# Performance work log

Hardware: AMD Instinct MI355X
Metric: run time of the kernel (lower is better)

The kernel has to match this reference:

```python
import jax, jax.numpy as jnp
import numpy as np

B, L, D, H = 2, 1000, 288, 8
DIM = D // H          # 36 per-head dim
DFF = 2 * D           # 576 conv-FFN hidden
KS = L // 4           # 250 sampled keys per query
NQ = L // 4           # 250 selected (active) queries
EPS = 1e-5


def _layernorm(x, g, b):
    mu = x.mean(-1, keepdims=True)
    var = ((x - mu) ** 2).mean(-1, keepdims=True)
    return (x - mu) * jax.lax.rsqrt(var + EPS) * g + b


def _prob_attention(q, k, v, index_key):
    # q,k,v: [b,h,L,dim]; index_key: [L, KS]
    b, h, l, dim = q.shape
    # sample KS keys per query row (gather): [b,h,L,KS,dim]
    k_samp = jnp.take(k, index_key, axis=2)
    # sampled scores: [b,h,L,KS]
    scores_samp = jnp.einsum('bhld,bhlkd->bhlk', q, k_samp)
    # sparsity measure M(q) = max - mean(over full l_key, as in source)
    measure = scores_samp.max(-1) - scores_samp.sum(-1) / l
    # top-NQ active queries per (b,h): [b,h,NQ]
    idx_q = jax.lax.top_k(measure, NQ)[1]
    q_sel = jnp.take_along_axis(q, idx_q[..., None], axis=2)  # [b,h,NQ,dim]
    sim = jnp.einsum('bhqd,bhkd->bhqk', q_sel, k) * (1.0 / np.sqrt(dim))
    attn = jax.nn.softmax(sim, axis=-1)
    out_sel = jnp.einsum('bhqk,bhkd->bhqd', attn, v)          # [b,h,NQ,dim]
    # lazy queries get mean(V); scatter active outputs in
    out = jnp.broadcast_to(v.mean(axis=2, keepdims=True), v.shape)
    bi = jnp.arange(b)[:, None, None]
    hi = jnp.arange(h)[None, :, None]
    out = out.at[bi, hi, idx_q].set(out_sel)
    return out  # [b,h,L,dim]


def reference(x, index_key, Wq, bq, Wk, bk, Wv, bv, W1, b1, W2, b2,
              ln1_g, ln1_b, ln2_g, ln2_b):
    b, l, d = x.shape
    # QKV projections -> [b,h,L,dim]
    q = (x @ Wq.T + bq).reshape(b, l, H, DIM).transpose(0, 2, 1, 3)
    k = (x @ Wk.T + bk).reshape(b, l, H, DIM).transpose(0, 2, 1, 3)
    v = (x @ Wv.T + bv).reshape(b, l, H, DIM).transpose(0, 2, 1, 3)
    attn = _prob_attention(q, k, v, index_key)
    attn = attn.transpose(0, 2, 1, 3).reshape(b, l, d)
    # residual + LN1 (dropout is identity in eval)
    h1 = _layernorm(x + attn, ln1_g, ln1_b)
    # conv FFN (kernel_size=1 conv == per-position linear), exact GELU
    f = jax.nn.gelu(h1 @ W1.T + b1, approximate=False)   # [b,l,DFF]
    f = jax.nn.gelu(f @ W2.T + b2, approximate=False)    # [b,l,d]
    return _layernorm(f + h1, ln2_g, ln2_b)


def setup_inputs() -> dict:
    key = jax.random.key(0)
    ks = jax.random.split(key, 10)
    s = 0.05
    return {
        'x': jax.random.normal(ks[0], (B, L, D), jnp.float32),
        'index_key': jax.random.randint(ks[1], (L, KS), 0, L),
        'Wq': jax.random.normal(ks[2], (D, D), jnp.float32) * s,
        'bq': jnp.zeros((D,), jnp.float32),
        'Wk': jax.random.normal(ks[3], (D, D), jnp.float32) * s,
        'bk': jnp.zeros((D,), jnp.float32),
        'Wv': jax.random.normal(ks[4], (D, D), jnp.float32) * s,
        'bv': jnp.zeros((D,), jnp.float32),
        'W1': jax.random.normal(ks[5], (DFF, D), jnp.float32) * s,
        'b1': jnp.zeros((DFF,), jnp.float32),
        'W2': jax.random.normal(ks[6], (D, DFF), jnp.float32) * s,
        'b2': jnp.zeros((D,), jnp.float32),
        'ln1_g': jnp.ones((D,), jnp.float32),
        'ln1_b': jnp.zeros((D,), jnp.float32),
        'ln2_g': jnp.ones((D,), jnp.float32),
        'ln2_b': jnp.zeros((D,), jnp.float32),
    }
```

## Files before the change

kernel.cpp:

```cpp
#include <hip/hip_runtime.h>
#include <math.h>

#define B_ 2
#define L_ 1000
#define D_ 288
#define H_ 8
#define DIM_ 36
#define DFF_ 576
#define KS_ 250
#define NQ_ 250
#define BH_ (B_ * H_)
#define EPS_ 1e-5f
#define PSTRIDE_ 40
#define MAXCL_ 125

__device__ __forceinline__ float gelu_exact(float x) {
    return 0.5f * x * (1.0f + erff(x * 0.70710678118654752f));
}

__device__ __forceinline__ float dot4(float4 a, float4 b) {
    return a.x * b.x + a.y * b.y + a.z * b.z + a.w * b.w;
}

__global__ __launch_bounds__(256) void qkv_transpose_kernel(
    const float* __restrict__ Wq, const float* __restrict__ Wk,
    const float* __restrict__ Wv,
    float* __restrict__ WqT, float* __restrict__ WkT, float* __restrict__ WvT)
{
    __shared__ float tile[32][33];
    const int m = blockIdx.x / 81;
    const int t = blockIdx.x % 81;
    const float* src = (m == 0) ? Wq : (m == 1) ? Wk : Wv;
    float* dst = (m == 0) ? WqT : (m == 1) ? WkT : WvT;
    const int ty0 = (t / 9) * 32, tx0 = (t % 9) * 32;
    const int tx = threadIdx.x & 31, ty = threadIdx.x >> 5;
#pragma unroll
    for (int i = 0; i < 4; i++)
        tile[ty + 8 * i][tx] = src[(size_t)(ty0 + ty + 8 * i) * D_ + tx0 + tx];
    __syncthreads();
#pragma unroll
    for (int i = 0; i < 4; i++)
        dst[(size_t)(tx0 + ty + 8 * i) * D_ + ty0 + tx] = tile[tx][ty + 8 * i];
}

__global__ __launch_bounds__(256) void ffn_transpose_kernel(
    const float* __restrict__ W1, const float* __restrict__ W2,
    float* __restrict__ W1T, float* __restrict__ W2T)
{
    __shared__ float tile[32][33];
    int t = blockIdx.x;
    const float* src; float* dst; int Rr, Cc, ntx;
    if (t < 162) { src = W1; dst = W1T; Rr = DFF_; Cc = D_; ntx = 9; }
    else { t -= 162; src = W2; dst = W2T; Rr = D_; Cc = DFF_; ntx = 18; }
    const int ty0 = (t / ntx) * 32, tx0 = (t % ntx) * 32;
    const int tx = threadIdx.x & 31, ty = threadIdx.x >> 5;
#pragma unroll
    for (int i = 0; i < 4; i++)
        tile[ty + 8 * i][tx] = src[(size_t)(ty0 + ty + 8 * i) * Cc + tx0 + tx];
    __syncthreads();
#pragma unroll
    for (int i = 0; i < 4; i++)
        dst[(size_t)(tx0 + ty + 8 * i) * Rr + ty0 + tx] = tile[tx][ty + 8 * i];
}

__global__ __launch_bounds__(256) void qkvT2_kernel(
    const float* __restrict__ x,
    const float* __restrict__ WqT, const float* __restrict__ WkT,
    const float* __restrict__ WvT,
    const float* __restrict__ bq, const float* __restrict__ bk,
    const float* __restrict__ bv,
    float* __restrict__ Q, float* __restrict__ K, float* __restrict__ V,
    float* __restrict__ KT)
{
    __shared__ float xsT[D_][4];
    const int base = blockIdx.x * 4;
    const int tid = threadIdx.x;

    for (int idx = tid; idx < 4 * D_; idx += 256) {
        int r = idx / D_, k = idx % D_;
        xsT[k][r] = x[(size_t)(base + r) * D_ + k];
    }
    __syncthreads();

    if (tid < 216) {
        const int gcol = 4 * tid;
        const int m = gcol / D_;
        const int c = gcol - m * D_;
        const float* WT = (m == 0) ? WqT : (m == 1) ? WkT : WvT;
        const float* bias = (m == 0) ? bq : (m == 1) ? bk : bv;
        float* outp = (m == 0) ? Q : (m == 1) ? K : V;

        float a[4][4];
#pragma unroll
        for (int j = 0; j < 4; j++) {
            float bv2 = bias[c + j];
#pragma unroll
            for (int r = 0; r < 4; r++) a[j][r] = bv2;
        }

        for (int k = 0; k < D_; k++) {
            float4 w = *(const float4*)(WT + (size_t)k * D_ + c);
            float4 xv = *(const float4*)&xsT[k][0];
            a[0][0] += w.x * xv.x; a[0][1] += w.x * xv.y; a[0][2] += w.x * xv.z; a[0][3] += w.x * xv.w;
            a[1][0] += w.y * xv.x; a[1][1] += w.y * xv.y; a[1][2] += w.y * xv.z; a[1][3] += w.y * xv.w;
            a[2][0] += w.z * xv.x; a[2][1] += w.z * xv.y; a[2][2] += w.z * xv.z; a[2][3] += w.z * xv.w;
            a[3][0] += w.w * xv.x; a[3][1] += w.w * xv.y; a[3][2] += w.w * xv.z; a[3][3] += w.w * xv.w;
        }

        const int bb_ = base / L_;
        const int l0 = base % L_;
#pragma unroll
        for (int j = 0; j < 4; j++) {
            int col = c + j;
            int h = col / DIM_, dd = col % DIM_;
#pragma unroll
            for (int r = 0; r < 4; r++) {
                int row = base + r;
                int b = row / L_, l = row % L_;
                outp[((size_t)(b * H_ + h) * L_ + l) * DIM_ + dd] = a[j][r];
            }
            if (m == 1) {
                *(float4*)(KT + ((size_t)(bb_ * H_ + h) * DIM_ + dd) * L_ + l0) =
                    make_float4(a[j][0], a[j][1], a[j][2], a[j][3]);
            }
        }
    }
}

__global__ __launch_bounds__(320) void qkv_kernel(
    const float* __restrict__ x,
    const float* __restrict__ Wq, const float* __restrict__ bq,
    const float* __restrict__ Wk, const float* __restrict__ bk,
    const float* __restrict__ Wv, const float* __restrict__ bv,
    float* __restrict__ Q, float* __restrict__ K, float* __restrict__ V)
{
    constexpr int R = 8;
    __shared__ float xs[R][D_];
    const int base = blockIdx.x * R;
    const int tid = threadIdx.x;

    const float4* xsrc = (const float4*)(x + (size_t)base * D_);
    float4* xdst = (float4*)&xs[0][0];
    for (int i = tid; i < R * D_ / 4; i += 320) xdst[i] = xsrc[i];
    __syncthreads();

    if (tid < D_) {
        const float4* wq4 = (const float4*)(Wq + (size_t)tid * D_);
        const float4* wk4 = (const float4*)(Wk + (size_t)tid * D_);
        const float4* wv4 = (const float4*)(Wv + (size_t)tid * D_);
        float aq[R], ak[R], av[R];
        float biasq = bq[tid], biask = bk[tid], biasv = bv[tid];
#pragma unroll
        for (int r = 0; r < R; r++) { aq[r] = biasq; ak[r] = biask; av[r] = biasv; }
        for (int d4 = 0; d4 < D_ / 4; d4++) {
            float4 wqv = wq4[d4], wkv = wk4[d4], wvv = wv4[d4];
#pragma unroll
            for (int r = 0; r < R; r++) {
                float4 hv = *(const float4*)&xs[r][d4 * 4];
                aq[r] += dot4(hv, wqv);
                ak[r] += dot4(hv, wkv);
                av[r] += dot4(hv, wvv);
            }
        }
        const int h = tid / DIM_, dd = tid % DIM_;
#pragma unroll
        for (int r = 0; r < R; r++) {
            int row = base + r;
            int b = row / L_, l = row % L_;
            size_t o = ((size_t)(b * H_ + h) * L_ + l) * DIM_ + dd;
            Q[o] = aq[r]; K[o] = ak[r]; V[o] = av[r];
        }
    }
}

__global__ __launch_bounds__(256) void score_measure3_kernel(
    const float* __restrict__ Q, const float* __restrict__ KT,
    const int* __restrict__ index_key, float* __restrict__ measure)
{
    constexpr int R = 8;
    __shared__ float qs[R][DIM_];
    __shared__ float st[R][1004];
    const int bh = blockIdx.x / 125;
    const int qt = blockIdx.x % 125;
    const int tid = threadIdx.x;

    if (tid < R * DIM_ / 4)
        ((float4*)&qs[0][0])[tid] =
            ((const float4*)(Q + ((size_t)bh * L_ + qt * R) * DIM_))[tid];
    __syncthreads();

    const float* KTb = KT + (size_t)bh * DIM_ * L_;
#pragma unroll
    for (int i = 0; i < 4; i++) {
        const int k = i * 256 + tid;
        if (k < L_) {
            float acc[R];
#pragma unroll
            for (int r = 0; r < R; r++) acc[r] = 0.f;
#pragma unroll
            for (int d4 = 0; d4 < DIM_ / 4; d4++) {
                float4 kv;
                kv.x = KTb[(size_t)(d4 * 4 + 0) * L_ + k];
                kv.y = KTb[(size_t)(d4 * 4 + 1) * L_ + k];
                kv.z = KTb[(size_t)(d4 * 4 + 2) * L_ + k];
                kv.w = KTb[(size_t)(d4 * 4 + 3) * L_ + k];
#pragma unroll
                for (int r = 0; r < R; r++)
                    acc[r] += dot4(*(const float4*)&qs[r][d4 * 4], kv);
            }
#pragma unroll
            for (int r = 0; r < R; r++) st[r][k] = acc[r];
        }
    }
    __syncthreads();

    const int r = tid >> 5;
    const int lane = tid & 31;
    const int l = qt * R + r;
    const int* ik = index_key + l * KS_;
    float mx = -1e30f, sm = 0.f;
    for (int s = lane; s < KS_; s += 32) {
        float v = st[r][ik[s]];
        mx = fmaxf(mx, v);
        sm += v;
    }
#pragma unroll
    for (int off = 16; off; off >>= 1) {
        mx = fmaxf(mx, __shfl_xor(mx, off));
        sm += __shfl_xor(sm, off);
    }
    if (lane == 0) measure[bh * L_ + l] = mx - sm * (1.0f / (float)L_);
}

__global__ __launch_bounds__(256) void measure_kernel(
    const float* __restrict__ Q, const float* __restrict__ K,
    const int* __restrict__ index_key, float* __restrict__ measure)
{
    const int w = threadIdx.x >> 6;
    const int lane = threadIdx.x & 63;
    const int wid = blockIdx.x * 4 + w;
    const int bh = wid / L_;
    const int l = wid % L_;

    const float4* qp = (const float4*)(Q + ((size_t)bh * L_ + l) * DIM_);
    float4 q[9];
#pragma unroll
    for (int i = 0; i < 9; i++) q[i] = qp[i];

    const int* ik = index_key + l * KS_;
    const float* Kb = K + (size_t)bh * L_ * DIM_;

    float mx = -1e30f, sm = 0.f;
#pragma unroll
    for (int s = lane; s < KS_; s += 64) {
        int kidx = ik[s];
        const float4* k4 = (const float4*)(Kb + (size_t)kidx * DIM_);
        float acc = 0.f;
#pragma unroll
        for (int i = 0; i < 9; i++) acc += dot4(q[i], k4[i]);
        mx = fmaxf(mx, acc);
        sm += acc;
    }
#pragma unroll
    for (int off = 32; off; off >>= 1) {
        mx = fmaxf(mx, __shfl_xor(mx, off));
        sm += __shfl_xor(sm, off);
    }
    if (lane == 0) measure[wid] = mx - sm * (1.0f / (float)L_);
}

__global__ __launch_bounds__(256) void topk_vmean_kernel(
    const float* __restrict__ measure, int* __restrict__ qlist,
    int* __restrict__ slot_map, const float* __restrict__ V,
    float* __restrict__ Vmean)
{
    if (blockIdx.x < BH_ * 4) {
        const int bh = blockIdx.x >> 2;
        const int quarter = blockIdx.x & 3;
        __shared__ float m[L_];
        for (int i = threadIdx.x; i < L_; i += 256) m[i] = measure[bh * L_ + i];
        __syncthreads();
        const int i = quarter * 250 + threadIdx.x;
        if (threadIdx.x < 250) {
            float mi = m[i];
            int rank = 0;
            for (int j = 0; j < L_; j++) {
                float mj = m[j];
                rank += (mj > mi) || (mj == mi && j < i);
            }
            if (rank < NQ_) qlist[bh * NQ_ + rank] = i;
            slot_map[bh * L_ + i] = (rank < NQ_) ? rank : -1;
        }
    } else {
        const int bh = blockIdx.x - BH_ * 4;
        const int tid = threadIdx.x;
        __shared__ float red2[7][DIM_];
        if (tid < 252) {
            int gq = tid / DIM_, d = tid % DIM_;
            const float* basep = V + (size_t)bh * L_ * DIM_;
            float s = 0.f;
            for (int l = gq; l < L_; l += 7) s += basep[l * DIM_ + d];
            red2[gq][d] = s;
        }
        __syncthreads();
        if (tid < DIM_) {
            float s = 0.f;
#pragma unroll
            for (int gq = 0; gq < 7; gq++) s += red2[gq][tid];
            Vmean[bh * DIM_ + tid] = s * (1.0f / L_);
        }
    }
}

__global__ __launch_bounds__(256) void attn_part2_kernel(
    const float* __restrict__ Q, const float* __restrict__ K,
    const float* __restrict__ V, const int* __restrict__ qlist,
    float* __restrict__ part, int nchunk, int chunk_len)
{
    __shared__ float Ks[MAXCL_ * DIM_];
    __shared__ float Vs[MAXCL_ * DIM_];
    const int bh = blockIdx.x / nchunk;
    const int chunk = blockIdx.x % nchunk;
    const int tid = threadIdx.x;
    const int k0 = chunk * chunk_len;

    {
        const float4* Ksrc = (const float4*)(K + ((size_t)bh * L_ + k0) * DIM_);
        const float4* Vsrc = (const float4*)(V + ((size_t)bh * L_ + k0) * DIM_);
        const int nf4 = chunk_len * (DIM_ / 4);
        for (int i = tid; i < nf4; i += 256) {
            ((float4*)Ks)[i] = Ksrc[i];
            ((float4*)Vs)[i] = Vsrc[i];
        }
    }
    __syncthreads();

    const int slot = tid;
    if (slot >= NQ_) return;

    const int qidx = qlist[bh * NQ_ + slot];
    const float4* qp = (const float4*)(Q + ((size_t)bh * L_ + qidx) * DIM_);
    float4 q[9];
#pragma unroll
    for (int i = 0; i < 9; i++) q[i] = qp[i];

    const float scale = (float)(1.0 / 6.0);
    float4 acc[9];
#pragma unroll
    for (int i = 0; i < 9; i++) acc[i] = make_float4(0.f, 0.f, 0.f, 0.f);
    float sum = 0.f;

    for (int j = 0; j < chunk_len; j++) {
        const float4* kp = (const float4*)(Ks + j * DIM_);
        float s = 0.f;
#pragma unroll
        for (int i = 0; i < 9; i++) s += dot4(q[i], kp[i]);
        float e = __expf(s * scale);
        sum += e;
        const float4* vp = (const float4*)(Vs + j * DIM_);
#pragma unroll
        for (int i = 0; i < 9; i++) {
            float4 vv = vp[i];
            acc[i].x += e * vv.x;
            acc[i].y += e * vv.y;
            acc[i].z += e * vv.z;
            acc[i].w += e * vv.w;
        }
    }

    float* p = part + ((size_t)(bh * NQ_ + slot) * nchunk + chunk) * PSTRIDE_;
#pragma unroll
    for (int i = 0; i < 9; i++) ((float4*)p)[i] = acc[i];
    p[DIM_] = sum;
}

__global__ __launch_bounds__(320) void combine_ln1_kernel(
    const float* __restrict__ x, const float* __restrict__ part,
    const int* __restrict__ slot_map, const float* __restrict__ Vmean,
    const float* __restrict__ g, const float* __restrict__ bb,
    float* __restrict__ h1, int nchunk)
{
    const int row = blockIdx.x;
    const int b = row / L_, l = row % L_;
    const int tid = threadIdx.x;
    __shared__ float psum[5], pssq[5];

    float y = 0.f;
    if (tid < D_) {
        const int h = tid / DIM_, d = tid % DIM_;
        const int bh = b * H_ + h;
        const int slot = slot_map[bh * L_ + l];
        float v;
        if (slot < 0) {
            v = Vmean[bh * DIM_ + d];
        } else {
            const float* p = part + (size_t)(bh * NQ_ + slot) * nchunk * PSTRIDE_;
            float a = 0.f, s = 0.f;
            for (int c = 0; c < nchunk; c++) {
                a += p[c * PSTRIDE_ + d];
                s += p[c * PSTRIDE_ + DIM_];
            }
            v = a / s;
        }
        y = x[(size_t)row * D_ + tid] + v;
    }

    float s1 = y, s2 = y * y;
#pragma unroll
    for (int off = 32; off; off >>= 1) {
        s1 += __shfl_xor(s1, off);
        s2 += __shfl_xor(s2, off);
    }
    const int w = tid >> 6, lane = tid & 63;
    if (lane == 0) { psum[w] = s1; pssq[w] = s2; }
    __syncthreads();
    float ts = 0.f, tq = 0.f;
#pragma unroll
    for (int i = 0; i < 5; i++) { ts += psum[i]; tq += pssq[i]; }
    float mu = ts * (1.0f / D_);
    float var = tq * (1.0f / D_) - mu * mu;
    float rstd = rsqrtf(var + EPS_);
    if (tid < D_)
        h1[(size_t)row * D_ + tid] = (y - mu) * rstd * g[tid] + bb[tid];
}

__global__ __launch_bounds__(288) void ffn_fused3_kernel(
    const float* __restrict__ h1,
    const float* __restrict__ W1T, const float* __restrict__ b1,
    const float* __restrict__ W2T, const float* __restrict__ b2,
    const float* __restrict__ g, const float* __restrict__ bb,
    float* __restrict__ out)
{
    constexpr int R = 8;
    __shared__ float hs[R][D_];
    __shared__ float fs[R][DFF_];
    __shared__ float red[6912];
    __shared__ float ys[R][D_];
    const int base = blockIdx.x * R;
    const int tid = threadIdx.x;

    {
        const float4* src = (const float4*)(h1 + (size_t)base * D_);
        float4* dst = (float4*)&hs[0][0];
        for (int i = tid; i < R * D_ / 4; i += 288) dst[i] = src[i];
    }
    __syncthreads();

    {
        const int kg = tid / 144;
        const int ct = tid - kg * 144;
        const int c = 4 * ct;
        float a[4][R];
#pragma unroll
        for (int j = 0; j < 4; j++) {
            float bv = (kg == 0) ? b1[c + j] : 0.f;
#pragma unroll
            for (int r = 0; r < R; r++) a[j][r] = bv;
        }
        const int kbeg = kg * 144;
        for (int k = kbeg; k < kbeg + 144; k++) {
            float4 w = *(const float4*)(W1T + (size_t)k * DFF_ + c);
#pragma unroll
            for (int r = 0; r < R; r++) {
                float xv = hs[r][k];
                a[0][r] += w.x * xv;
                a[1][r] += w.y * xv;
                a[2][r] += w.z * xv;
                a[3][r] += w.w * xv;
            }
        }
        if (kg == 1) {
#pragma unroll
            for (int j = 0; j < 4; j++) {
                *(float4*)&red[(j * 144 + ct) * 8 + 0] =
                    make_float4(a[j][0], a[j][1], a[j][2], a[j][3]);
                *(float4*)&red[(j * 144 + ct) * 8 + 4] =
                    make_float4(a[j][4], a[j][5], a[j][6], a[j][7]);
            }
        }
        __syncthreads();
        if (kg == 0) {
            float y[4][R];
#pragma unroll
            for (int j = 0; j < 4; j++) {
                float4 o0 = *(const float4*)&red[(j * 144 + ct) * 8 + 0];
                float4 o1 = *(const float4*)&red[(j * 144 + ct) * 8 + 4];
                y[j][0] = gelu_exact(a[j][0] + o0.x);
                y[j][1] = gelu_exact(a[j][1] + o0.y);
                y[j][2] = gelu_exact(a[j][2] + o0.z);
                y[j][3] = gelu_exact(a[j][3] + o0.w);
                y[j][4] = gelu_exact(a[j][4] + o1.x);
                y[j][5] = gelu_exact(a[j][5] + o1.y);
                y[j][6] = gelu_exact(a[j][6] + o1.z);
                y[j][7] = gelu_exact(a[j][7] + o1.w);
            }
#pragma unroll
            for (int r = 0; r < R; r++)
                *(float4*)&fs[r][c] = make_float4(y[0][r], y[1][r], y[2][r], y[3][r]);
        }
    }
    __syncthreads();

    {
        const int kg = tid / 72;
        const int ct = tid - kg * 72;
        const int c = 4 * ct;
        float a[4][R];
#pragma unroll
        for (int j = 0; j < 4; j++) {
            float bv = (kg == 0) ? b2[c + j] : 0.f;
#pragma unroll
            for (int r = 0; r < R; r++) a[j][r] = bv;
        }
        const int kbeg = kg * 144;
        for (int k = kbeg; k < kbeg + 144; k++) {
            float4 w = *(const float4*)(W2T + (size_t)k * D_ + c);
#pragma unroll
            for (int r = 0; r < R; r++) {
                float fv = fs[r][k];
                a[0][r] += w.x * fv;
                a[1][r] += w.y * fv;
                a[2][r] += w.z * fv;
                a[3][r] += w.w * fv;
            }
        }
        if (kg >= 1) {
#pragma unroll
            for (int j = 0; j < 4; j++) {
                *(float4*)&red[(((kg - 1) * 4 + j) * 72 + ct) * 8 + 0] =
                    make_float4(a[j][0], a[j][1], a[j][2], a[j][3]);
                *(float4*)&red[(((kg - 1) * 4 + j) * 72 + ct) * 8 + 4] =
                    make_float4(a[j][4], a[j][5], a[j][6], a[j][7]);
            }
        }
        __syncthreads();
        if (kg == 0) {
            float y[4][R];
#pragma unroll
            for (int j = 0; j < 4; j++) {
#pragma unroll
                for (int rq = 0; rq < 2; rq++) {
                    float4 o0 = *(const float4*)&red[((0 * 4 + j) * 72 + ct) * 8 + rq * 4];
                    float4 o1 = *(const float4*)&red[((1 * 4 + j) * 72 + ct) * 8 + rq * 4];
                    float4 o2 = *(const float4*)&red[((2 * 4 + j) * 72 + ct) * 8 + rq * 4];
                    y[j][rq * 4 + 0] = gelu_exact(a[j][rq * 4 + 0] + o0.x + o1.x + o2.x) + hs[rq * 4 + 0][c + j];
                    y[j][rq * 4 + 1] = gelu_exact(a[j][rq * 4 + 1] + o0.y + o1.y + o2.y) + hs[rq * 4 + 1][c + j];
                    y[j][rq * 4 + 2] = gelu_exact(a[j][rq * 4 + 2] + o0.z + o1.z + o2.z) + hs[rq * 4 + 2][c + j];
                    y[j][rq * 4 + 3] = gelu_exact(a[j][rq * 4 + 3] + o0.w + o1.w + o2.w) + hs[rq * 4 + 3][c + j];
                }
            }
#pragma unroll
            for (int r = 0; r < R; r++)
                *(float4*)&ys[r][c] = make_float4(y[0][r], y[1][r], y[2][r], y[3][r]);
        }
    }
    __syncthreads();

    const int w = tid >> 6;
    const int lane = tid & 63;
    if (w < 4) {
#pragma unroll
        for (int rr = 0; rr < 2; rr++) {
            const int r = w * 2 + rr;
            float s = 0.f, ss = 0.f;
#pragma unroll
            for (int i = 0; i < 5; i++) {
                int j = lane + i * 64;
                if (j < D_) { float yv = ys[r][j]; s += yv; ss += yv * yv; }
            }
#pragma unroll
            for (int off = 32; off; off >>= 1) {
                s += __shfl_xor(s, off);
                ss += __shfl_xor(ss, off);
            }
            float mu = s * (1.0f / D_);
            float var = ss * (1.0f / D_) - mu * mu;
            float rstd = rsqrtf(var + EPS_);
            int row = base + r;
#pragma unroll
            for (int i = 0; i < 5; i++) {
                int j = lane + i * 64;
                if (j < D_)
                    out[(size_t)row * D_ + j] = (ys[r][j] - mu) * rstd * g[j] + bb[j];
            }
        }
    }
}

__global__ __launch_bounds__(192) void ffn1_kernel(
    const float* __restrict__ h1,
    const float* __restrict__ W1, const float* __restrict__ b1,
    float* __restrict__ f1)
{
    constexpr int R = 8;
    __shared__ float hs[R][D_];
    const int base = blockIdx.x * R;
    const int tid = threadIdx.x;

    const float4* hsrc = (const float4*)(h1 + (size_t)base * D_);
    float4* hdst = (float4*)&hs[0][0];
    for (int i = tid; i < R * D_ / 4; i += 192) hdst[i] = hsrc[i];
    __syncthreads();

    const int j0 = tid, j1 = tid + 192, j2 = tid + 384;
    const float4* w0 = (const float4*)(W1 + (size_t)j0 * D_);
    const float4* w1 = (const float4*)(W1 + (size_t)j1 * D_);
    const float4* w2 = (const float4*)(W1 + (size_t)j2 * D_);
    float a0[R], a1[R], a2[R];
    float bb0 = b1[j0], bb1 = b1[j1], bb2 = b1[j2];
#pragma unroll
    for (int r = 0; r < R; r++) { a0[r] = bb0; a1[r] = bb1; a2[r] = bb2; }

    for (int d4 = 0; d4 < D_ / 4; d4++) {
        float4 x0 = w0[d4], x1 = w1[d4], x2 = w2[d4];
#pragma unroll
        for (int r = 0; r < R; r++) {
            float4 hv = *(const float4*)&hs[r][d4 * 4];
            a0[r] += dot4(hv, x0);
            a1[r] += dot4(hv, x1);
            a2[r] += dot4(hv, x2);
        }
    }
#pragma unroll
    for (int r = 0; r < R; r++) {
        size_t rowo = (size_t)(base + r) * DFF_;
        f1[rowo + j0] = gelu_exact(a0[r]);
        f1[rowo + j1] = gelu_exact(a1[r]);
        f1[rowo + j2] = gelu_exact(a2[r]);
    }
}

__global__ __launch_bounds__(320) void ffn2_ln_kernel(
    const float* __restrict__ f1, const float* __restrict__ h1,
    const float* __restrict__ W2, const float* __restrict__ b2,
    const float* __restrict__ g, const float* __restrict__ bb,
    float* __restrict__ out)
{
    constexpr int R = 8;
    __shared__ float fs[R][DFF_];
    __shared__ float hs[R][D_];
    __shared__ float ys[R][D_];
    const int base = blockIdx.x * R;
    const int tid = threadIdx.x;

    const float4* fsrc = (const float4*)(f1 + (size_t)base * DFF_);
    float4* fdst = (float4*)&fs[0][0];
    for (int i = tid; i < R * DFF_ / 4; i += 320) fdst[i] = fsrc[i];
    const float4* hsrc = (const float4*)(h1 + (size_t)base * D_);
    float4* hdst = (float4*)&hs[0][0];
    for (int i = tid; i < R * D_ / 4; i += 320) hdst[i] = hsrc[i];
    __syncthreads();

    if (tid < D_) {
        const float4* w4 = (const float4*)(W2 + (size_t)tid * DFF_);
        float acc[R];
        float bias = b2[tid];
#pragma unroll
        for (int r = 0; r < R; r++) acc[r] = bias;
        for (int d4 = 0; d4 < DFF_ / 4; d4++) {
            float4 wv = w4[d4];
#pragma unroll
            for (int r = 0; r < R; r++) {
                float4 fv = *(const float4*)&fs[r][d4 * 4];
                acc[r] += dot4(fv, wv);
            }
        }
#pragma unroll
        for (int r = 0; r < R; r++) ys[r][tid] = gelu_exact(acc[r]) + hs[r][tid];
    }
    __syncthreads();

    const int w = tid >> 6;
    const int lane = tid & 63;
    for (int r = w; r < R; r += 5) {
        float s = 0.f, ss = 0.f;
#pragma unroll
        for (int i = 0; i < 5; i++) {
            int j = lane + i * 64;
            if (j < D_) { float y = ys[r][j]; s += y; ss += y * y; }
        }
#pragma unroll
        for (int off = 32; off; off >>= 1) {
            s += __shfl_xor(s, off);
            ss += __shfl_xor(ss, off);
        }
        float mu = s * (1.0f / D_);
        float var = ss * (1.0f / D_) - mu * mu;
        float rstd = rsqrtf(var + EPS_);
        int row = base + r;
#pragma unroll
        for (int i = 0; i < 5; i++) {
            int j = lane + i * 64;
            if (j < D_) out[(size_t)row * D_ + j] = (ys[r][j] - mu) * rstd * g[j] + bb[j];
        }
    }
}

extern "C" void kernel_launch(void* const* d_in, const int* in_sizes, int n_in,
                              void* d_out, int out_size, void* d_ws, size_t ws_size,
                              hipStream_t stream)
{
    const float* x         = (const float*)d_in[0];
    const int*   index_key = (const int*)  d_in[1];
    const float* Wq = (const float*)d_in[2];
    const float* bq = (const float*)d_in[3];
    const float* Wk = (const float*)d_in[4];
    const float* bk = (const float*)d_in[5];
    const float* Wv = (const float*)d_in[6];
    const float* bv = (const float*)d_in[7];
    const float* W1 = (const float*)d_in[8];
    const float* b1 = (const float*)d_in[9];
    const float* W2 = (const float*)d_in[10];
    const float* b2 = (const float*)d_in[11];
    const float* ln1_g = (const float*)d_in[12];
    const float* ln1_b = (const float*)d_in[13];
    const float* ln2_g = (const float*)d_in[14];
    const float* ln2_b = (const float*)d_in[15];
    float* out = (float*)d_out;

    float* Q        = (float*)d_ws;
    float* K        = Q + 576000;
    float* V        = K + 576000;
    float* Vmean    = V + 576000;
    float* measure  = Vmean + 576;
    float* attn_out = measure + 16000;
    float* h1       = attn_out + 576000;
    int*   qlist    = (int*)(h1 + 576000);
    int*   slot_map = qlist + 4000;
    float* part     = (float*)(slot_map + 16000);
    float* f1       = part;
    float* KT       = part + 4000000;

    float* WqT = part;
    float* WkT = WqT + 82944;
    float* WvT = WkT + 82944;
    float* W1T = part;
    float* W2T = part + 165888;

    const size_t kt_end = 2916576ull + 4000000ull + 576000ull;
    const bool   big    = ws_size >= kt_end * sizeof(float);
    const int    nchunk = big ? 25 : 8;
    const int    chunk_len = L_ / nchunk;

    if (big) {
        qkv_transpose_kernel<<<243, 256, 0, stream>>>(Wq, Wk, Wv, WqT, WkT, WvT);
        qkvT2_kernel<<<500, 256, 0, stream>>>(x, WqT, WkT, WvT, bq, bk, bv, Q, K, V, KT);
        score_measure3_kernel<<<BH_ * 125, 256, 0, stream>>>(Q, KT, index_key, measure);
    } else {
        qkv_kernel<<<250, 320, 0, stream>>>(x, Wq, bq, Wk, bk, Wv, bv, Q, K, V);
        measure_kernel<<<4000, 256, 0, stream>>>(Q, K, index_key, measure);
    }
    topk_vmean_kernel<<<BH_ * 4 + BH_, 256, 0, stream>>>(measure, qlist, slot_map, V, Vmean);
    attn_part2_kernel<<<BH_ * nchunk, 256, 0, stream>>>(Q, K, V, qlist, part, nchunk, chunk_len);
    combine_ln1_kernel<<<B_ * L_, 320, 0, stream>>>(x, part, slot_map, Vmean,
                                                    ln1_g, ln1_b, h1, nchunk);
    if (big) {
        ffn_transpose_kernel<<<324, 256, 0, stream>>>(W1, W2, W1T, W2T);
        ffn_fused3_kernel<<<250, 288, 0, stream>>>(h1, W1T, b1, W2T, b2, ln2_g, ln2_b, out);
    } else {
        ffn1_kernel<<<250, 192, 0, stream>>>(h1, W1, b1, f1);
        ffn2_ln_kernel<<<250, 320, 0, stream>>>(f1, h1, W2, b2, ln2_g, ln2_b, out);
    }
}
```

Baseline: 273.2 us.

## Merge weight transposes into one launch and split-K the QKV and FFN kernels

All five weight transposes now run in a single prep kernel, and the FFN weights are written to a separate buffer so they are no longer overwritten by the attention partials. The QKV projection splits its K loop across two thread groups (448 threads) and reduces the halves through shared memory. The fused FFN kernel processes 4 rows per block instead of 8, with 576 threads and a 4-way split-K for the first GEMM, giving twice as many blocks. The intent is more parallelism and one fewer launch, at the cost of extra shared-memory reductions, more barriers, and less weight reuse per block.

```diff
diff --git a/kernel.cpp b/kernel.cpp
--- a/kernel.cpp
+++ b/kernel.cpp
@@ -22,48 +22,45 @@
     return a.x * b.x + a.y * b.y + a.z * b.z + a.w * b.w;
 }
 
-__global__ __launch_bounds__(256) void qkv_transpose_kernel(
+__global__ __launch_bounds__(256) void weights_prep_kernel(
     const float* __restrict__ Wq, const float* __restrict__ Wk,
     const float* __restrict__ Wv,
-    float* __restrict__ WqT, float* __restrict__ WkT, float* __restrict__ WvT)
-{
-    __shared__ float tile[32][33];
-    const int m = blockIdx.x / 81;
-    const int t = blockIdx.x % 81;
-    const float* src = (m == 0) ? Wq : (m == 1) ? Wk : Wv;
-    float* dst = (m == 0) ? WqT : (m == 1) ? WkT : WvT;
-    const int ty0 = (t / 9) * 32, tx0 = (t % 9) * 32;
-    const int tx = threadIdx.x & 31, ty = threadIdx.x >> 5;
-#pragma unroll
-    for (int i = 0; i < 4; i++)
-        tile[ty + 8 * i][tx] = src[(size_t)(ty0 + ty + 8 * i) * D_ + tx0 + tx];
-    __syncthreads();
-#pragma unroll
-    for (int i = 0; i < 4; i++)
-        dst[(size_t)(tx0 + ty + 8 * i) * D_ + ty0 + tx] = tile[tx][ty + 8 * i];
-}
-
-__global__ __launch_bounds__(256) void ffn_transpose_kernel(
+    float* __restrict__ WqT, float* __restrict__ WkT, float* __restrict__ WvT,
     const float* __restrict__ W1, const float* __restrict__ W2,
     float* __restrict__ W1T, float* __restrict__ W2T)
 {
     __shared__ float tile[32][33];
-    int t = blockIdx.x;
-    const float* src; float* dst; int Rr, Cc, ntx;
-    if (t < 162) { src = W1; dst = W1T; Rr = DFF_; Cc = D_; ntx = 9; }
-    else { t -= 162; src = W2; dst = W2T; Rr = D_; Cc = DFF_; ntx = 18; }
-    const int ty0 = (t / ntx) * 32, tx0 = (t % ntx) * 32;
     const int tx = threadIdx.x & 31, ty = threadIdx.x >> 5;
-#pragma unroll
-    for (int i = 0; i < 4; i++)
-        tile[ty + 8 * i][tx] = src[(size_t)(ty0 + ty + 8 * i) * Cc + tx0 + tx];
-    __syncthreads();
-#pragma unroll
-    for (int i = 0; i < 4; i++)
-        dst[(size_t)(tx0 + ty + 8 * i) * Rr + ty0 + tx] = tile[tx][ty + 8 * i];
-}
-
-__global__ __launch_bounds__(256) void qkvT2_kernel(
+    if (blockIdx.x < 243) {
+        const int m = blockIdx.x / 81;
+        const int t = blockIdx.x % 81;
+        const float* src = (m == 0) ? Wq : (m == 1) ? Wk : Wv;
+        float* dst = (m == 0) ? WqT : (m == 1) ? WkT : WvT;
+        const int ty0 = (t / 9) * 32, tx0 = (t % 9) * 32;
+#pragma unroll
+        for (int i = 0; i < 4; i++)
+            tile[ty + 8 * i][tx] = src[(size_t)(ty0 + ty + 8 * i) * D_ + tx0 + tx];
+        __syncthreads();
+#pragma unroll
+        for (int i = 0; i < 4; i++)
+            dst[(size_t)(tx0 + ty + 8 * i) * D_ + ty0 + tx] = tile[tx][ty + 8 * i];
+    } else {
+        int t = blockIdx.x - 243;
+        const float* src; float* dst; int Rr, Cc, ntx;
+        if (t < 162) { src = W1; dst = W1T; Rr = DFF_; Cc = D_; ntx = 9; }
+        else { t -= 162; src = W2; dst = W2T; Rr = D_; Cc = DFF_; ntx = 18; }
+        const int ty0 = (t / ntx) * 32, tx0 = (t % ntx) * 32;
+#pragma unroll
+        for (int i = 0; i < 4; i++)
+            tile[ty + 8 * i][tx] = src[(size_t)(ty0 + ty + 8 * i) * Cc + tx0 + tx];
+        __syncthreads();
+#pragma unroll
+        for (int i = 0; i < 4; i++)
+            dst[(size_t)(tx0 + ty + 8 * i) * Rr + ty0 + tx] = tile[tx][ty + 8 * i];
+    }
+}
+
+__global__ __launch_bounds__(448) void qkvT3_kernel(
     const float* __restrict__ x,
     const float* __restrict__ WqT, const float* __restrict__ WkT,
     const float* __restrict__ WvT,
@@ -73,32 +70,37 @@
     float* __restrict__ KT)
 {
     __shared__ float xsT[D_][4];
+    __shared__ float red[3456];
     const int base = blockIdx.x * 4;
     const int tid = threadIdx.x;
 
-    for (int idx = tid; idx < 4 * D_; idx += 256) {
+    for (int idx = tid; idx < 4 * D_; idx += 448) {
         int r = idx / D_, k = idx % D_;
         xsT[k][r] = x[(size_t)(base + r) * D_ + k];
     }
     __syncthreads();
 
-    if (tid < 216) {
-        const int gcol = 4 * tid;
-        const int m = gcol / D_;
-        const int c = gcol - m * D_;
-        const float* WT = (m == 0) ? WqT : (m == 1) ? WkT : WvT;
+    const int kg = tid / 216;
+    const int ct = tid - kg * 216;
+    const bool active = tid < 432;
+
+    float a[4][4];
+    const float* WT = nullptr;
+    int m = 0, c = 0;
+    if (active) {
+        const int gcol = 4 * ct;
+        m = gcol / D_;
+        c = gcol - m * D_;
+        WT = (m == 0) ? WqT : (m == 1) ? WkT : WvT;
         const float* bias = (m == 0) ? bq : (m == 1) ? bk : bv;
-        float* outp = (m == 0) ? Q : (m == 1) ? K : V;
-
-        float a[4][4];
 #pragma unroll
         for (int j = 0; j < 4; j++) {
-            float bv2 = bias[c + j];
+            float bv2 = (kg == 0) ? bias[c + j] : 0.f;
 #pragma unroll
             for (int r = 0; r < 4; r++) a[j][r] = bv2;
         }
-
-        for (int k = 0; k < D_; k++) {
+        const int kbeg = kg * 144;
+        for (int k = kbeg; k < kbeg + 144; k++) {
             float4 w = *(const float4*)(WT + (size_t)k * D_ + c);
             float4 xv = *(const float4*)&xsT[k][0];
             a[0][0] += w.x * xv.x; a[0][1] += w.x * xv.y; a[0][2] += w.x * xv.z; a[0][3] += w.x * xv.w;
@@ -106,11 +108,23 @@
             a[2][0] += w.z * xv.x; a[2][1] += w.z * xv.y; a[2][2] += w.z * xv.z; a[2][3] += w.z * xv.w;
             a[3][0] += w.w * xv.x; a[3][1] += w.w * xv.y; a[3][2] += w.w * xv.z; a[3][3] += w.w * xv.w;
         }
-
+        if (kg == 1) {
+#pragma unroll
+            for (int j = 0; j < 4; j++)
+                *(float4*)&red[(j * 216 + ct) * 4] =
+                    make_float4(a[j][0], a[j][1], a[j][2], a[j][3]);
+        }
+    }
+    __syncthreads();
+
+    if (active && kg == 0) {
         const int bb_ = base / L_;
         const int l0 = base % L_;
+        float* outp = (m == 0) ? Q : (m == 1) ? K : V;
 #pragma unroll
         for (int j = 0; j < 4; j++) {
+            float4 o = *(const float4*)&red[(j * 216 + ct) * 4];
+            a[j][0] += o.x; a[j][1] += o.y; a[j][2] += o.z; a[j][3] += o.w;
             int col = c + j;
             int h = col / DIM_, dd = col % DIM_;
 #pragma unroll
@@ -424,25 +438,24 @@
         h1[(size_t)row * D_ + tid] = (y - mu) * rstd * g[tid] + bb[tid];
 }
 
-__global__ __launch_bounds__(288) void ffn_fused3_kernel(
+__global__ __launch_bounds__(576) void ffn_fused4_kernel(
     const float* __restrict__ h1,
     const float* __restrict__ W1T, const float* __restrict__ b1,
     const float* __restrict__ W2T, const float* __restrict__ b2,
     const float* __restrict__ g, const float* __restrict__ bb,
     float* __restrict__ out)
 {
-    constexpr int R = 8;
-    __shared__ float hs[R][D_];
-    __shared__ float fs[R][DFF_];
-    __shared__ float red[6912];
+    constexpr int R = 4;
+    __shared__ float hsT[D_][R];
+    __shared__ float fsT[DFF_][R];
+    __shared__ float red[8064];
     __shared__ float ys[R][D_];
     const int base = blockIdx.x * R;
     const int tid = threadIdx.x;
 
-    {
-        const float4* src = (const float4*)(h1 + (size_t)base * D_);
-        float4* dst = (float4*)&hs[0][0];
-        for (int i = tid; i < R * D_ / 4; i += 288) dst[i] = src[i];
+    for (int idx = tid; idx < R * D_; idx += 576) {
+        int r = idx / D_, k = idx % D_;
+        hsT[k][r] = h1[(size_t)(base + r) * D_ + k];
     }
     __syncthreads();
 
@@ -450,53 +463,41 @@
         const int kg = tid / 144;
         const int ct = tid - kg * 144;
         const int c = 4 * ct;
-        float a[4][R];
+        float a[4][4];
 #pragma unroll
         for (int j = 0; j < 4; j++) {
             float bv = (kg == 0) ? b1[c + j] : 0.f;
 #pragma unroll
-            for (int r = 0; r < R; r++) a[j][r] = bv;
-        }
-        const int kbeg = kg * 144;
-        for (int k = kbeg; k < kbeg + 144; k++) {
+            for (int r = 0; r < 4; r++) a[j][r] = bv;
+        }
+        const int kbeg = kg * 72;
+        for (int k = kbeg; k < kbeg + 72; k++) {
             float4 w = *(const float4*)(W1T + (size_t)k * DFF_ + c);
-#pragma unroll
-            for (int r = 0; r < R; r++) {
-                float xv = hs[r][k];
-                a[0][r] += w.x * xv;
-                a[1][r] += w.y * xv;
-                a[2][r] += w.z * xv;
-                a[3][r] += w.w * xv;
-            }
-        }
-        if (kg == 1) {
-#pragma unroll
-            for (int j = 0; j < 4; j++) {
-                *(float4*)&red[(j * 144 + ct) * 8 + 0] =
+            float4 xv = *(const float4*)&hsT[k][0];
+            a[0][0] += w.x * xv.x; a[0][1] += w.x * xv.y; a[0][2] += w.x * xv.z; a[0][3] += w.x * xv.w;
+            a[1][0] += w.y * xv.x; a[1][1] += w.y * xv.y; a[1][2] += w.y * xv.z; a[1][3] += w.y * xv.w;
+            a[2][0] += w.z * xv.x; a[2][1] += w.z * xv.y; a[2][2] += w.z * xv.z; a[2][3] += w.z * xv.w;
+            a[3][0] += w.w * xv.x; a[3][1] += w.w * xv.y; a[3][2] += w.w * xv.z; a[3][3] += w.w * xv.w;
+        }
+        if (kg >= 1) {
+#pragma unroll
+            for (int j = 0; j < 4; j++)
+                *(float4*)&red[(((kg - 1) * 576) + j * 144 + ct) * 4] =
                     make_float4(a[j][0], a[j][1], a[j][2], a[j][3]);
-                *(float4*)&red[(j * 144 + ct) * 8 + 4] =
-                    make_float4(a[j][4], a[j][5], a[j][6], a[j][7]);
-            }
         }
         __syncthreads();
         if (kg == 0) {
-            float y[4][R];
 #pragma unroll
             for (int j = 0; j < 4; j++) {
-                float4 o0 = *(const float4*)&red[(j * 144 + ct) * 8 + 0];
-                float4 o1 = *(const float4*)&red[(j * 144 + ct) * 8 + 4];
-                y[j][0] = gelu_exact(a[j][0] + o0.x);
-                y[j][1] = gelu_exact(a[j][1] + o0.y);
-                y[j][2] = gelu_exact(a[j][2] + o0.z);
-                y[j][3] = gelu_exact(a[j][3] + o0.w);
-                y[j][4] = gelu_exact(a[j][4] + o1.x);
-                y[j][5] = gelu_exact(a[j][5] + o1.y);
-                y[j][6] = gelu_exact(a[j][6] + o1.z);
-                y[j][7] = gelu_exact(a[j][7] + o1.w);
-            }
-#pragma unroll
-            for (int r = 0; r < R; r++)
-                *(float4*)&fs[r][c] = make_float4(y[0][r], y[1][r], y[2][r], y[3][r]);
+                float4 o0 = *(const float4*)&red[((0 * 576) + j * 144 + ct) * 4];
+                float4 o1 = *(const float4*)&red[((1 * 576) + j * 144 + ct) * 4];
+                float4 o2 = *(const float4*)&red[((2 * 576) + j * 144 + ct) * 4];
+                float y0 = gelu_exact(a[j][0] + o0.x + o1.x + o2.x);
+                float y1 = gelu_exact(a[j][1] + o0.y + o1.y + o2.y);
+                float y2 = gelu_exact(a[j][2] + o0.z + o1.z + o2.z);
+                float y3 = gelu_exact(a[j][3] + o0.w + o1.w + o2.w);
+                *(float4*)&fsT[c + j][0] = make_float4(y0, y1, y2, y3);
+            }
         }
     }
     __syncthreads();
@@ -505,52 +506,47 @@
         const int kg = tid / 72;
         const int ct = tid - kg * 72;
         const int c = 4 * ct;
-        float a[4][R];
+        float a[4][4];
 #pragma unroll
         for (int j = 0; j < 4; j++) {
             float bv = (kg == 0) ? b2[c + j] : 0.f;
 #pragma unroll
-            for (int r = 0; r < R; r++) a[j][r] = bv;
-        }
-        const int kbeg = kg * 144;
-        for (int k = kbeg; k < kbeg + 144; k++) {
+            for (int r = 0; r < 4; r++) a[j][r] = bv;
+        }
+        const int kbeg = kg * 72;
+        for (int k = kbeg; k < kbeg + 72; k++) {
             float4 w = *(const float4*)(W2T + (size_t)k * D_ + c);
-#pragma unroll
-            for (int r = 0; r < R; r++) {
-                float fv = fs[r][k];
-                a[0][r] += w.x * fv;
-                a[1][r] += w.y * fv;
-                a[2][r] += w.z * fv;
-                a[3][r] += w.w * fv;
-            }
+            float4 fv = *(const float4*)&fsT[k][0];
+            a[0][0] += w.x * fv.x; a[0][1] += w.x * fv.y; a[0][2] += w.x * fv.z; a[0][3] += w.x * fv.w;
+            a[1][0] += w.y * fv.x; a[1][1] += w.y * fv.y; a[1][2] += w.y * fv.z; a[1][3] += w.y * fv.w;
+            a[2][0] += w.z * fv.x; a[2][1] += w.z * fv.y; a[2][2] += w.z * fv.z; a[2][3] += w.z * fv.w;
+            a[3][0] += w.w * fv.x; a[3][1] += w.w * fv.y; a[3][2] += w.w * fv.z; a[3][3] += w.w * fv.w;
         }
         if (kg >= 1) {
 #pragma unroll
-            for (int j = 0; j < 4; j++) {
-                *(float4*)&red[(((kg - 1) * 4 + j) * 72 + ct) * 8 + 0] =
+            for (int j = 0; j < 4; j++)
+                *(float4*)&red[(((kg - 1) * 288) + j * 72 + ct) * 4] =
                     make_float4(a[j][0], a[j][1], a[j][2], a[j][3]);
-                *(float4*)&red[(((kg - 1) * 4 + j) * 72 + ct) * 8 + 4] =
-                    make_float4(a[j][4], a[j][5], a[j][6], a[j][7]);
-            }
         }
         __syncthreads();
         if (kg == 0) {
-            float y[4][R];
+            float y[4][4];
 #pragma unroll
             for (int j = 0; j < 4; j++) {
-#pragma unroll
-                for (int rq = 0; rq < 2; rq++) {
-                    float4 o0 = *(const float4*)&red[((0 * 4 + j) * 72 + ct) * 8 + rq * 4];
-                    float4 o1 = *(const float4*)&red[((1 * 4 + j) * 72 + ct) * 8 + rq * 4];
-                    float4 o2 = *(const float4*)&red[((2 * 4 + j) * 72 + ct) * 8 + rq * 4];
-                    y[j][rq * 4 + 0] = gelu_exact(a[j][rq * 4 + 0] + o0.x + o1.x + o2.x) + hs[rq * 4 + 0][c + j];
-                    y[j][rq * 4 + 1] = gelu_exact(a[j][rq * 4 + 1] + o0.y + o1.y + o2.y) + hs[rq * 4 + 1][c + j];
-                    y[j][rq * 4 + 2] = gelu_exact(a[j][rq * 4 + 2] + o0.z + o1.z + o2.z) + hs[rq * 4 + 2][c + j];
-                    y[j][rq * 4 + 3] = gelu_exact(a[j][rq * 4 + 3] + o0.w + o1.w + o2.w) + hs[rq * 4 + 3][c + j];
+                float t0 = a[j][0], t1 = a[j][1], t2 = a[j][2], t3 = a[j][3];
+#pragma unroll
+                for (int kk = 0; kk < 7; kk++) {
+                    float4 o = *(const float4*)&red[((kk * 288) + j * 72 + ct) * 4];
+                    t0 += o.x; t1 += o.y; t2 += o.z; t3 += o.w;
                 }
-            }
-#pragma unroll
-            for (int r = 0; r < R; r++)
+                float4 hres = *(const float4*)&hsT[c + j][0];
+                y[j][0] = gelu_exact(t0) + hres.x;
+                y[j][1] = gelu_exact(t1) + hres.y;
+                y[j][2] = gelu_exact(t2) + hres.z;
+                y[j][3] = gelu_exact(t3) + hres.w;
+            }
+#pragma unroll
+            for (int r = 0; r < 4; r++)
                 *(float4*)&ys[r][c] = make_float4(y[0][r], y[1][r], y[2][r], y[3][r]);
         }
     }
@@ -559,30 +555,27 @@
     const int w = tid >> 6;
     const int lane = tid & 63;
     if (w < 4) {
-#pragma unroll
-        for (int rr = 0; rr < 2; rr++) {
-            const int r = w * 2 + rr;
-            float s = 0.f, ss = 0.f;
-#pragma unroll
-            for (int i = 0; i < 5; i++) {
-                int j = lane + i * 64;
-                if (j < D_) { float yv = ys[r][j]; s += yv; ss += yv * yv; }
-            }
-#pragma unroll
-            for (int off = 32; off; off >>= 1) {
-                s += __shfl_xor(s, off);
-                ss += __shfl_xor(ss, off);
-            }
-            float mu = s * (1.0f / D_);
-            float var = ss * (1.0f / D_) - mu * mu;
-            float rstd = rsqrtf(var + EPS_);
-            int row = base + r;
-#pragma unroll
-            for (int i = 0; i < 5; i++) {
-                int j = lane + i * 64;
-                if (j < D_)
-                    out[(size_t)row * D_ + j] = (ys[r][j] - mu) * rstd * g[j] + bb[j];
-            }
+        const int r = w;
+        float s = 0.f, ss = 0.f;
+#pragma unroll
+        for (int i = 0; i < 5; i++) {
+            int j = lane + i * 64;
+            if (j < D_) { float yv = ys[r][j]; s += yv; ss += yv * yv; }
+        }
+#pragma unroll
+        for (int off = 32; off; off >>= 1) {
+            s += __shfl_xor(s, off);
+            ss += __shfl_xor(ss, off);
+        }
+        float mu = s * (1.0f / D_);
+        float var = ss * (1.0f / D_) - mu * mu;
+        float rstd = rsqrtf(var + EPS_);
+        int row = base + r;
+#pragma unroll
+        for (int i = 0; i < 5; i++) {
+            int j = lane + i * 64;
+            if (j < D_)
+                out[(size_t)row * D_ + j] = (ys[r][j] - mu) * rstd * g[j] + bb[j];
         }
     }
 }
@@ -723,8 +716,8 @@
     float* V        = K + 576000;
     float* Vmean    = V + 576000;
     float* measure  = Vmean + 576;
-    float* attn_out = measure + 16000;
-    float* h1       = attn_out + 576000;
+    float* wtbuf    = measure + 16000;
+    float* h1       = wtbuf + 576000;
     int*   qlist    = (int*)(h1 + 576000);
     int*   slot_map = qlist + 4000;
     float* part     = (float*)(slot_map + 16000);
@@ -734,8 +727,8 @@
     float* WqT = part;
     float* WkT = WqT + 82944;
     float* WvT = WkT + 82944;
-    float* W1T = part;
-    float* W2T = part + 165888;
+    float* W1T = wtbuf;
+    float* W2T = wtbuf + 165888;
 
     const size_t kt_end = 2916576ull + 4000000ull + 576000ull;
     const bool   big    = ws_size >= kt_end * sizeof(float);
@@ -743,8 +736,10 @@
     const int    chunk_len = L_ / nchunk;
 
     if (big) {
-        qkv_transpose_kernel<<<243, 256, 0, stream>>>(Wq, Wk, Wv, WqT, WkT, WvT);
-        qkvT2_kernel<<<500, 256, 0, stream>>>(x, WqT, WkT, WvT, bq, bk, bv, Q, K, V, KT);
+        weights_prep_kernel<<<567, 256, 0, stream>>>(Wq, Wk, Wv, WqT, WkT, WvT,
+                                                     W1, W2, W1T, W2T);
+        qkvT3_kernel<<<500, 448, 0, stream>>>(x, WqT, WkT, WvT, bq, bk, bv,
+                                              Q, K, V, KT);
         score_measure3_kernel<<<BH_ * 125, 256, 0, stream>>>(Q, KT, index_key, measure);
     } else {
         qkv_kernel<<<250, 320, 0, stream>>>(x, Wq, bq, Wk, bk, Wv, bv, Q, K, V);
@@ -755,8 +750,8 @@
     combine_ln1_kernel<<<B_ * L_, 320, 0, stream>>>(x, part, slot_map, Vmean,
                                                     ln1_g, ln1_b, h1, nchunk);
     if (big) {
-        ffn_transpose_kernel<<<324, 256, 0, stream>>>(W1, W2, W1T, W2T);
-        ffn_fused3_kernel<<<250, 288, 0, stream>>>(h1, W1T, b1, W2T, b2, ln2_g, ln2_b, out);
+        ffn_fused4_kernel<<<500, 576, 0, stream>>>(h1, W1T, b1, W2T, b2,
+                                                   ln2_g, ln2_b, out);
     } else {
         ffn1_kernel<<<250, 192, 0, stream>>>(h1, W1, b1, f1);
         ffn2_ln_kernel<<<250, 320, 0, stream>>>(f1, h1, W2, b2, ln2_g, ln2_b, out);
```

After: 253.8 us. 1.08x faster.
